# Kernel optimization log

Hardware: AMD Instinct MI355X
Metric: run time of the kernel (lower is better)

The kernel has to match this reference:

```python
import jax, jax.numpy as jnp
import numpy as np

N_IN = 100000
N_OUT = 200000
C_IN = 128
C_OUT = 64
K = 27  # 3x3x3 kernel offsets
M = 100000  # neighbor-map pairs per kernel offset
BN_EPS = 1e-5


def setup_inputs() -> dict:
    key = jax.random.key(0)
    k1, k2, k3, k4 = jax.random.split(key, 4)
    x = jax.random.normal(k1, (N_IN, C_IN), dtype=jnp.float32)
    weight = jax.random.normal(k2, (K, C_IN, C_OUT), dtype=jnp.float32) * (1.0 / np.sqrt(C_IN * K))
    gamma = jnp.ones((C_OUT,), dtype=jnp.float32)
    beta = jnp.zeros((C_OUT,), dtype=jnp.float32)
    in_map = jax.random.randint(k3, (K, M), 0, N_IN, dtype=jnp.int32)
    out_map = jax.random.randint(k4, (K, M), 0, N_OUT, dtype=jnp.int32)
    return {"x": x, "weight": weight, "gamma": gamma, "beta": beta,
            "in_map": in_map, "out_map": out_map}


def sparse_transposed_conv(x, weight, in_map, out_map):
    # gather-GEMM-scatter over K kernel offsets (torchsparse semantics)
    out = jnp.zeros((N_OUT, C_OUT), dtype=x.dtype)

    def body(k, out):
        gathered = x[in_map[k]]                # [M, C_in] irregular gather
        contrib = gathered @ weight[k]         # [M, C_out] small GEMM
        return out.at[out_map[k]].add(contrib) # irregular scatter-add

    return jax.lax.fori_loop(0, K, body, out)


def reference(x, weight, gamma, beta, in_map, out_map):
    out = sparse_transposed_conv(x, weight, in_map, out_map)
    # BatchNorm over points (training-mode batch statistics, biased var)
    mean = jnp.mean(out, axis=0)
    var = jnp.mean(jnp.square(out - mean), axis=0)
    y = (out - mean) * (gamma * jax.lax.rsqrt(var + BN_EPS)) + beta
    return jnp.maximum(y, 0.0)  # ReLU
```

## Files before the change

### kernel.cpp

```cpp
#include <hip/hip_runtime.h>
#include <hip/hip_fp16.h>

#define N_IN   100000
#define N_OUT  200000
#define C_IN   128
#define C_OUT  64
#define NK     27
#define MM     100000
#define BN_EPS 1e-5f

#define TILE_M 128
#define APAD   136

typedef short bf16x8 __attribute__((ext_vector_type(8)));
typedef float f32x4  __attribute__((ext_vector_type(4)));

__device__ __forceinline__ unsigned pack2_bf16(float a, float b) {
  unsigned ua = __float_as_uint(a);
  unsigned ub = __float_as_uint(b);
  ua = (ua + 0x7FFFu + ((ua >> 16) & 1u)) >> 16;
  ub = (ub + 0x7FFFu + ((ub >> 16) & 1u)) & 0xFFFF0000u;
  return ua | ub;
}

__device__ __forceinline__ unsigned pack2_f16(float lo, float hi) {
  __half2 h = __floats2half2_rn(lo, hi);
  return *(unsigned*)&h;
}

__device__ __forceinline__ void pk_atomic_f16(const void* addr, unsigned pw) {
  asm volatile("global_atomic_pk_add_f16 %0, %1, off"
               :: "v"((unsigned long long)addr), "v"(pw) : "memory");
}

__global__ void convert_kernel(const float* __restrict__ x, unsigned* __restrict__ xb,
                               const float* __restrict__ w, unsigned* __restrict__ wt) {
  if (blockIdx.x < 6250) {
    int id = blockIdx.x * 256 + threadIdx.x;
    const float4* xs = (const float4*)x;
    float4 v0 = xs[2 * id];
    float4 v1 = xs[2 * id + 1];
    uint4 o;
    o.x = pack2_bf16(v0.x, v0.y);
    o.y = pack2_bf16(v0.z, v0.w);
    o.z = pack2_bf16(v1.x, v1.y);
    o.w = pack2_bf16(v1.z, v1.w);
    ((uint4*)xb)[id] = o;
  } else {
    int pidx = (blockIdx.x - 6250) * 256 + threadIdx.x;
    int k   = pidx >> 12;
    int rem = pidx & 4095;
    int co  = rem >> 6;
    int ci0 = (rem & 63) * 2;
    const float* wk = w + (size_t)k * C_IN * C_OUT;
    float a = wk[ci0 * C_OUT + co];
    float b = wk[(ci0 + 1) * C_OUT + co];
    wt[pidx] = pack2_bf16(a, b);
  }
}

__global__ __launch_bounds__(256, 4) void scatter3_kernel(
    const uint4* __restrict__ xb,
    const unsigned short* __restrict__ wt,
    const int* __restrict__ in_map,
    const int* __restrict__ out_map,
    unsigned short* __restrict__ acc16)
{
  __shared__ unsigned short Bls[C_OUT * APAD];

  const int t = threadIdx.x;
  const int k = blockIdx.y;
  const int mbase = blockIdx.x * TILE_M;

  {
    const uint4* src = (const uint4*)(wt + (size_t)k * C_OUT * C_IN);
    #pragma unroll
    for (int i = 0; i < 4; ++i) {
      int ch  = t + i * 256;
      int co  = ch >> 4;
      int ci0 = (ch & 15) * 8;
      *(uint4*)&Bls[co * APAD + ci0] = src[ch];
    }
  }

  const int wave = t >> 6;
  const int lane = t & 63;
  const int quad = lane >> 4;
  const int l15  = lane & 15;
  const int rb   = wave * 32;

  const int m0 = mbase + rb + l15;
  const int m1 = m0 + 16;
  const int src0 = (m0 < MM) ? in_map[k * MM + m0] : 0;
  const int src1 = (m1 < MM) ? in_map[k * MM + m1] : 0;
  const uint4* xr0 = xb + (size_t)src0 * 16 + quad;
  const uint4* xr1 = xb + (size_t)src1 * 16 + quad;
  uint4 a0[4], a1[4];
  #pragma unroll
  for (int kk = 0; kk < 4; ++kk) {
    a0[kk] = xr0[kk * 4];
    a1[kk] = xr1[kk * 4];
  }

  __syncthreads();

  f32x4 acc[2][4];
  #pragma unroll
  for (int i = 0; i < 2; ++i)
    #pragma unroll
    for (int j = 0; j < 4; ++j)
      acc[i][j] = (f32x4){0.f, 0.f, 0.f, 0.f};

  #pragma unroll
  for (int kk = 0; kk < 4; ++kk) {
    const int koff = kk * 32 + quad * 8;
    bf16x8 fa0 = *(const bf16x8*)&a0[kk];
    bf16x8 fa1 = *(const bf16x8*)&a1[kk];
    bf16x8 b0 = *(const bf16x8*)&Bls[(l15) * APAD + koff];
    bf16x8 b1 = *(const bf16x8*)&Bls[(16 + l15) * APAD + koff];
    bf16x8 b2 = *(const bf16x8*)&Bls[(32 + l15) * APAD + koff];
    bf16x8 b3 = *(const bf16x8*)&Bls[(48 + l15) * APAD + koff];
    acc[0][0] = __builtin_amdgcn_mfma_f32_16x16x32_bf16(fa0, b0, acc[0][0], 0, 0, 0);
    acc[0][1] = __builtin_amdgcn_mfma_f32_16x16x32_bf16(fa0, b1, acc[0][1], 0, 0, 0);
    acc[0][2] = __builtin_amdgcn_mfma_f32_16x16x32_bf16(fa0, b2, acc[0][2], 0, 0, 0);
    acc[0][3] = __builtin_amdgcn_mfma_f32_16x16x32_bf16(fa0, b3, acc[0][3], 0, 0, 0);
    acc[1][0] = __builtin_amdgcn_mfma_f32_16x16x32_bf16(fa1, b0, acc[1][0], 0, 0, 0);
    acc[1][1] = __builtin_amdgcn_mfma_f32_16x16x32_bf16(fa1, b1, acc[1][1], 0, 0, 0);
    acc[1][2] = __builtin_amdgcn_mfma_f32_16x16x32_bf16(fa1, b2, acc[1][2], 0, 0, 0);
    acc[1][3] = __builtin_amdgcn_mfma_f32_16x16x32_bf16(fa1, b3, acc[1][3], 0, 0, 0);
  }

  const int par = l15 & 1;
  #pragma unroll
  for (int rt = 0; rt < 2; ++rt) {
    int rloc = rb + rt * 16 + quad * 4;
    int mrow = mbase + rloc;
    int4 o4;
    if (mrow + 3 < MM) {
      o4 = *(const int4*)(out_map + (size_t)k * MM + mrow);
    } else {
      o4.x = (mrow + 0 < MM) ? out_map[(size_t)k * MM + mrow + 0] : 0;
      o4.y = (mrow + 1 < MM) ? out_map[(size_t)k * MM + mrow + 1] : 0;
      o4.z = (mrow + 2 < MM) ? out_map[(size_t)k * MM + mrow + 2] : 0;
      o4.w = (mrow + 3 < MM) ? out_map[(size_t)k * MM + mrow + 3] : 0;
    }
    int om4[4] = {o4.x, o4.y, o4.z, o4.w};
    #pragma unroll
    for (int ct = 0; ct < 4; ++ct) {
      f32x4 v = acc[rt][ct];
      int colb = ct * 16 + (l15 & ~1);
      #pragma unroll
      for (int i = 0; i < 4; ++i) {
        float vn = __shfl_xor(v[i], 1);
        float lo = par ? vn : v[i];
        float hi = par ? v[i] : vn;
        unsigned pw = pack2_f16(lo, hi);
        if (((i & 1) == par) && (mrow + i < MM)) {
          const unsigned short* addr = acc16 + (size_t)om4[i] * C_OUT + colb;
          pk_atomic_f16(addr, pw);
        }
      }
    }
  }
}

__global__ __launch_bounds__(256) void scatter_f32_kernel(
    const float* __restrict__ x,
    const unsigned short* __restrict__ wt,
    const int* __restrict__ in_map,
    const int* __restrict__ out_map,
    float* __restrict__ outf)
{
  __shared__ unsigned short Als[TILE_M * APAD];
  __shared__ unsigned short Bls[C_OUT * APAD];
  __shared__ int om[TILE_M];

  const int t = threadIdx.x;
  const int k = blockIdx.y;
  const int mbase = blockIdx.x * TILE_M;

  if (t < TILE_M) {
    int m = mbase + t;
    om[t] = (m < MM) ? out_map[k * MM + m] : 0;
  }
  {
    const uint4* src = (const uint4*)(wt + (size_t)k * C_OUT * C_IN);
    #pragma unroll
    for (int i = 0; i < 4; ++i) {
      int ch  = t + i * 256;
      int co  = ch >> 4;
      int ci0 = (ch & 15) * 8;
      *(uint4*)&Bls[co * APAD + ci0] = src[ch];
    }
  }
  {
    int r    = t >> 1;
    int half = t & 1;
    int m    = mbase + r;
    int src  = (m < MM) ? in_map[k * MM + m] : 0;
    const float4* xr = (const float4*)(x + (size_t)src * C_IN) + half * 16;
    uint2* dst = (uint2*)&Als[r * APAD + half * 64];
    #pragma unroll
    for (int j = 0; j < 16; ++j) {
      float4 v = xr[j];
      dst[j] = make_uint2(pack2_bf16(v.x, v.y), pack2_bf16(v.z, v.w));
    }
  }
  __syncthreads();

  const int wave = t >> 6;
  const int lane = t & 63;
  const int quad = lane >> 4;
  const int l15  = lane & 15;
  const int rb   = wave * 32;

  f32x4 acc[2][4];
  #pragma unroll
  for (int i = 0; i < 2; ++i)
    #pragma unroll
    for (int j = 0; j < 4; ++j)
      acc[i][j] = (f32x4){0.f, 0.f, 0.f, 0.f};

  #pragma unroll
  for (int kk = 0; kk < 4; ++kk) {
    const int koff = kk * 32 + quad * 8;
    bf16x8 a0 = *(const bf16x8*)&Als[(rb + l15) * APAD + koff];
    bf16x8 a1 = *(const bf16x8*)&Als[(rb + 16 + l15) * APAD + koff];
    bf16x8 b0 = *(const bf16x8*)&Bls[(l15) * APAD + koff];
    bf16x8 b1 = *(const bf16x8*)&Bls[(16 + l15) * APAD + koff];
    bf16x8 b2 = *(const bf16x8*)&Bls[(32 + l15) * APAD + koff];
    bf16x8 b3 = *(const bf16x8*)&Bls[(48 + l15) * APAD + koff];
    acc[0][0] = __builtin_amdgcn_mfma_f32_16x16x32_bf16(a0, b0, acc[0][0], 0, 0, 0);
    acc[0][1] = __builtin_amdgcn_mfma_f32_16x16x32_bf16(a0, b1, acc[0][1], 0, 0, 0);
    acc[0][2] = __builtin_amdgcn_mfma_f32_16x16x32_bf16(a0, b2, acc[0][2], 0, 0, 0);
    acc[0][3] = __builtin_amdgcn_mfma_f32_16x16x32_bf16(a0, b3, acc[0][3], 0, 0, 0);
    acc[1][0] = __builtin_amdgcn_mfma_f32_16x16x32_bf16(a1, b0, acc[1][0], 0, 0, 0);
    acc[1][1] = __builtin_amdgcn_mfma_f32_16x16x32_bf16(a1, b1, acc[1][1], 0, 0, 0);
    acc[1][2] = __builtin_amdgcn_mfma_f32_16x16x32_bf16(a1, b2, acc[1][2], 0, 0, 0);
    acc[1][3] = __builtin_amdgcn_mfma_f32_16x16x32_bf16(a1, b3, acc[1][3], 0, 0, 0);
  }

  #pragma unroll
  for (int rt = 0; rt < 2; ++rt) {
    int rloc = rb + rt * 16 + quad * 4;
    int4 o4 = *(const int4*)&om[rloc];
    int mrow = mbase + rloc;
    #pragma unroll
    for (int ct = 0; ct < 4; ++ct) {
      f32x4 v = acc[rt][ct];
      int col = ct * 16 + l15;
      if (mrow + 0 < MM) unsafeAtomicAdd(&outf[(size_t)o4.x * C_OUT + col], v[0]);
      if (mrow + 1 < MM) unsafeAtomicAdd(&outf[(size_t)o4.y * C_OUT + col], v[1]);
      if (mrow + 2 < MM) unsafeAtomicAdd(&outf[(size_t)o4.z * C_OUT + col], v[2]);
      if (mrow + 3 < MM) unsafeAtomicAdd(&outf[(size_t)o4.w * C_OUT + col], v[3]);
    }
  }
}

__global__ __launch_bounds__(256) void stats16_kernel(const unsigned* __restrict__ acc,
                                                      float* __restrict__ ws) {
  __shared__ float red[4][8][32];
  int t = threadIdx.x;
  int w = t & 31, sub = t >> 5;
  float s0 = 0, q0 = 0, s1 = 0, q1 = 0;
  for (int r = blockIdx.x * 8 + sub; r < N_OUT; r += gridDim.x * 8) {
    unsigned u = acc[(size_t)r * 32 + w];
    __half2 h = *(__half2*)&u;
    float a = __low2float(h), b = __high2float(h);
    s0 += a; q0 += a * a; s1 += b; q1 += b * b;
  }
  red[0][sub][w] = s0; red[1][sub][w] = q0;
  red[2][sub][w] = s1; red[3][sub][w] = q1;
  __syncthreads();
  if (t < 32) {
    float S0 = 0, Q0 = 0, S1 = 0, Q1 = 0;
    #pragma unroll
    for (int s = 0; s < 8; ++s) {
      S0 += red[0][s][t]; Q0 += red[1][s][t];
      S1 += red[2][s][t]; Q1 += red[3][s][t];
    }
    unsafeAtomicAdd(&ws[2 * t],      S0);
    unsafeAtomicAdd(&ws[64 + 2 * t], Q0);
    unsafeAtomicAdd(&ws[2 * t + 1],      S1);
    unsafeAtomicAdd(&ws[64 + 2 * t + 1], Q1);
  }
}

__global__ void finalize16_kernel(const uint2* __restrict__ acc,
                                  float* __restrict__ out,
                                  const float* __restrict__ ws) {
  int i = blockIdx.x * 256 + threadIdx.x;
  uint2 u = acc[i];
  __half2 h0 = *(__half2*)&u.x;
  __half2 h1 = *(__half2*)&u.y;
  int c0 = (i & 15) * 4;
  float s0 = ws[128 + c0], s1 = ws[129 + c0], s2 = ws[130 + c0], s3 = ws[131 + c0];
  float b0 = ws[192 + c0], b1 = ws[193 + c0], b2 = ws[194 + c0], b3 = ws[195 + c0];
  float4 v;
  v.x = fmaxf(fmaf(__low2float(h0),  s0, b0), 0.f);
  v.y = fmaxf(fmaf(__high2float(h0), s1, b1), 0.f);
  v.z = fmaxf(fmaf(__low2float(h1),  s2, b2), 0.f);
  v.w = fmaxf(fmaf(__high2float(h1), s3, b3), 0.f);
  ((float4*)out)[i] = v;
}

__global__ void stats_kernel(const float* __restrict__ out, float* __restrict__ ws) {
  __shared__ float ls[4][64];
  __shared__ float ls2[4][64];
  int t = threadIdx.x;
  int c = t & 63, sub = t >> 6;
  float s = 0.f, s2 = 0.f;
  for (int r = blockIdx.x * 4 + sub; r < N_OUT; r += gridDim.x * 4) {
    float v = out[(size_t)r * C_OUT + c];
    s += v; s2 += v * v;
  }
  ls[sub][c] = s; ls2[sub][c] = s2;
  __syncthreads();
  if (t < 64) {
    float ts = ls[0][t] + ls[1][t] + ls[2][t] + ls[3][t];
    float t2 = ls2[0][t] + ls2[1][t] + ls2[2][t] + ls2[3][t];
    unsafeAtomicAdd(&ws[t], ts);
    unsafeAtomicAdd(&ws[64 + t], t2);
  }
}

__global__ void finalize_kernel(float* __restrict__ out, const float* __restrict__ ws) {
  int i = blockIdx.x * 256 + threadIdx.x;
  float4 v = ((const float4*)out)[i];
  int c0 = (i & 15) * 4;
  float s0 = ws[128 + c0], s1 = ws[129 + c0], s2 = ws[130 + c0], s3 = ws[131 + c0];
  float b0 = ws[192 + c0], b1 = ws[193 + c0], b2 = ws[194 + c0], b3 = ws[195 + c0];
  v.x = fmaxf(fmaf(v.x, s0, b0), 0.f);
  v.y = fmaxf(fmaf(v.y, s1, b1), 0.f);
  v.z = fmaxf(fmaf(v.z, s2, b2), 0.f);
  v.w = fmaxf(fmaf(v.w, s3, b3), 0.f);
  ((float4*)out)[i] = v;
}

__global__ void prep_kernel(float* __restrict__ ws,
                            const float* __restrict__ gamma,
                            const float* __restrict__ beta) {
  int c = threadIdx.x;
  float mean = ws[c] * (1.0f / N_OUT);
  float var  = ws[64 + c] * (1.0f / N_OUT) - mean * mean;
  var = fmaxf(var, 0.0f);
  float sc = gamma[c] * rsqrtf(var + BN_EPS);
  ws[128 + c] = sc;
  ws[192 + c] = beta[c] - mean * sc;
}

extern "C" void kernel_launch(void* const* d_in, const int* in_sizes, int n_in,
                              void* d_out, int out_size, void* d_ws, size_t ws_size,
                              hipStream_t stream) {
  const float* x      = (const float*)d_in[0];
  const float* weight = (const float*)d_in[1];
  const float* gamma  = (const float*)d_in[2];
  const float* beta   = (const float*)d_in[3];
  const int* in_map   = (const int*)d_in[4];
  const int* out_map  = (const int*)d_in[5];
  float* out   = (float*)d_out;
  float* stats = (float*)d_ws;

  const size_t WT_OFF  = 4096;
  const size_t XB_OFF  = 1u << 20;
  const size_t XB_SZ   = (size_t)N_IN * C_IN * 2;
  const size_t ACC_OFF = XB_OFF + XB_SZ;
  const size_t ACC_SZ  = (size_t)N_OUT * C_OUT * 2;

  unsigned* wt = (unsigned*)((char*)d_ws + WT_OFF);
  unsigned* xb = (unsigned*)((char*)d_ws + XB_OFF);
  unsigned short* acc16 = (unsigned short*)((char*)d_ws + ACC_OFF);

  dim3 g((MM + TILE_M - 1) / TILE_M, NK);
  hipMemsetAsync(d_ws, 0, 1024, stream);

  if (ws_size >= ACC_OFF + ACC_SZ) {
    hipMemsetAsync(acc16, 0, ACC_SZ, stream);
    convert_kernel<<<6682, 256, 0, stream>>>(x, xb, weight, wt);
    scatter3_kernel<<<g, 256, 0, stream>>>((const uint4*)xb, (const unsigned short*)wt,
                                           in_map, out_map, acc16);
    stats16_kernel<<<1024, 256, 0, stream>>>((const unsigned*)acc16, stats);
    prep_kernel<<<1, 64, 0, stream>>>(stats, gamma, beta);
    finalize16_kernel<<<(N_OUT * C_OUT / 4 + 255) / 256, 256, 0, stream>>>(
        (const uint2*)acc16, out, stats);
  } else {
    hipMemsetAsync(d_out, 0, (size_t)N_OUT * C_OUT * sizeof(float), stream);
    convert_kernel<<<6682, 256, 0, stream>>>(x, xb, weight, wt);
    scatter_f32_kernel<<<g, 256, 0, stream>>>(x, (const unsigned short*)wt,
                                              in_map, out_map, out);
    stats_kernel<<<512, 256, 0, stream>>>(out, stats);
    prep_kernel<<<1, 64, 0, stream>>>(stats, gamma, beta);
    finalize_kernel<<<(N_OUT * C_OUT / 4 + 255) / 256, 256, 0, stream>>>(out, stats);
  }
}
```

Measured before the change: 730.7 us.

## Bucket neighbor pairs by output tile and accumulate in LDS before global atomics

Adds a counting-sort pipeline (histogram, per-tile scan, record scatter) that groups gather/scatter pairs by output tile of 100 rows and kernel offset. A new conv kernel then runs MFMA on 16-row chunks, accumulates into an fp32 LDS tile with workgroup atomics, and flushes once per slice with packed f16 global atomics. This is meant to replace many scattered global f16 atomics with LDS atomics plus fewer coalesced global atomics. The cost is several extra kernels and memsets, a large record buffer, and a fixed per-tile capacity that could overflow if the outputs are unevenly distributed.

After: 1.385 ms. 1.9x slower.

```diff
diff --git a/kernel.cpp b/kernel.cpp
--- a/kernel.cpp
+++ b/kernel.cpp
@@ -12,6 +12,13 @@
 #define TILE_M 128
 #define APAD   136
 
+#define TILE_R 100
+#define NTILE  2000
+#define NSLICE 4
+#define CAP_T  2048
+#define LROW   65
+#define CHCAP  128
+
 typedef short bf16x8 __attribute__((ext_vector_type(8)));
 typedef float f32x4  __attribute__((ext_vector_type(4)));
 
@@ -34,8 +41,9 @@
 }
 
 __global__ void convert_kernel(const float* __restrict__ x, unsigned* __restrict__ xb,
-                               const float* __restrict__ w, unsigned* __restrict__ wt) {
-  if (blockIdx.x < 6250) {
+                               const float* __restrict__ w, unsigned* __restrict__ wt,
+                               unsigned* __restrict__ wt2, int xblocks) {
+  if ((int)blockIdx.x < xblocks) {
     int id = blockIdx.x * 256 + threadIdx.x;
     const float4* xs = (const float4*)x;
     float4 v0 = xs[2 * id];
@@ -47,15 +55,167 @@
     o.w = pack2_bf16(v1.z, v1.w);
     ((uint4*)xb)[id] = o;
   } else {
-    int pidx = (blockIdx.x - 6250) * 256 + threadIdx.x;
+    int pidx = (blockIdx.x - xblocks) * 256 + threadIdx.x;
     int k   = pidx >> 12;
-    int rem = pidx & 4095;
-    int co  = rem >> 6;
-    int ci0 = (rem & 63) * 2;
     const float* wk = w + (size_t)k * C_IN * C_OUT;
-    float a = wk[ci0 * C_OUT + co];
-    float b = wk[(ci0 + 1) * C_OUT + co];
-    wt[pidx] = pack2_bf16(a, b);
+    {
+      int rem = pidx & 4095;
+      int co  = rem >> 6;
+      int ci0 = (rem & 63) * 2;
+      wt[pidx] = pack2_bf16(wk[ci0 * C_OUT + co], wk[(ci0 + 1) * C_OUT + co]);
+    }
+    {
+      int p     = pidx & 3;
+      int lane6 = (pidx >> 2) & 63;
+      int kk    = (pidx >> 8) & 3;
+      int ct    = (pidx >> 10) & 3;
+      int co  = ct * 16 + (lane6 & 15);
+      int ci0 = kk * 32 + (lane6 >> 4) * 8 + p * 2;
+      wt2[pidx] = pack2_bf16(wk[ci0 * C_OUT + co], wk[(ci0 + 1) * C_OUT + co]);
+    }
+  }
+}
+
+__global__ void hist_kernel(const int* __restrict__ out_map, int* __restrict__ cnt) {
+  int m = blockIdx.x * 256 + threadIdx.x;
+  int k = blockIdx.y;
+  if (m < MM) {
+    int o = out_map[k * MM + m];
+    atomicAdd(&cnt[(o / TILE_R) * NK + k], 1);
+  }
+}
+
+__global__ void tile_scan_kernel(const int* __restrict__ cnt,
+                                 int* __restrict__ off,
+                                 int* __restrict__ cur) {
+  int tile = blockIdx.x * 4 + (threadIdx.x >> 6);
+  int lane = threadIdx.x & 63;
+  if (tile >= NTILE) return;
+  int c = 0;
+  if (lane < NK) c = (cnt[tile * NK + lane] + 15) & ~15;
+  int p = c;
+  #pragma unroll
+  for (int d = 1; d < 32; d <<= 1) {
+    int n = __shfl_up(p, d);
+    if (lane >= d) p += n;
+  }
+  int base = tile * CAP_T + p - c;
+  if (lane < NK) { off[tile * 28 + lane] = base; cur[tile * 28 + lane] = base; }
+  if (lane == NK - 1) off[tile * 28 + NK] = base + c;
+}
+
+__global__ void scatter_rec_kernel(const int* __restrict__ in_map,
+                                   const int* __restrict__ out_map,
+                                   int* __restrict__ cur,
+                                   unsigned* __restrict__ rec) {
+  int m = blockIdx.x * 256 + threadIdx.x;
+  int k = blockIdx.y;
+  if (m < MM) {
+    int o = out_map[k * MM + m];
+    int tile = o / TILE_R;
+    int ol = o - tile * TILE_R;
+    int pos = atomicAdd(&cur[tile * 28 + k], 1);
+    rec[pos] = ((unsigned)in_map[k * MM + m] << 7) | (unsigned)ol;
+  }
+}
+
+__global__ __launch_bounds__(256) void conv_slice_kernel(
+    const uint4* __restrict__ xb,
+    const uint4* __restrict__ wt2,
+    const unsigned* __restrict__ rec,
+    const int* __restrict__ off,
+    unsigned short* __restrict__ acc16)
+{
+  __shared__ float Lacc[TILE_R * LROW];
+  __shared__ int chtab[CHCAP];
+  __shared__ int nch_s;
+
+  const int t     = threadIdx.x;
+  const int tile  = blockIdx.x >> 2;
+  const int slice = blockIdx.x & 3;
+  const int wave  = t >> 6;
+  const int lane  = t & 63;
+  const int quad  = lane >> 4;
+  const int l15   = lane & 15;
+
+  for (int i = t; i < TILE_R * LROW; i += 256) Lacc[i] = 0.f;
+
+  if (wave == 0) {
+    int cnt = 0, s0 = 0;
+    if (lane < NK) {
+      s0  = off[tile * 28 + lane];
+      cnt = (off[tile * 28 + lane + 1] - s0) >> 4;
+    }
+    int pos = cnt;
+    #pragma unroll
+    for (int d = 1; d < 32; d <<= 1) {
+      int n = __shfl_up(pos, d);
+      if (lane >= d) pos += n;
+    }
+    int base = pos - cnt;
+    for (int i = 0; i < cnt; ++i)
+      chtab[base + i] = (lane << 24) | ((s0 + (i << 4)) & 0xFFFFFF);
+    if (lane == NK - 1) nch_s = pos;
+  }
+  __syncthreads();
+
+  const int nch = nch_s;
+  const int cs  = (nch * slice) >> 2;
+  const int ce  = (nch * (slice + 1)) >> 2;
+
+  int kcur = -1;
+  bf16x8 B[4][4];
+
+  for (int ci = cs + wave; ci < ce; ci += 4) {
+    unsigned ent = (unsigned)chtab[ci];
+    const int k = (int)(ent >> 24);
+    unsigned r0 = rec[(ent & 0xFFFFFFu) + l15];
+    if (k != kcur) {
+      kcur = k;
+      const uint4* wkp = wt2 + (size_t)k * 1024 + lane;
+      #pragma unroll
+      for (int ct = 0; ct < 4; ++ct)
+        #pragma unroll
+        for (int kk = 0; kk < 4; ++kk)
+          B[ct][kk] = *(const bf16x8*)(wkp + (ct * 4 + kk) * 64);
+    }
+    unsigned row0 = (r0 & 0x80000000u) ? 0u : (r0 >> 7);
+    uint4 a[4];
+    #pragma unroll
+    for (int kk = 0; kk < 4; ++kk) a[kk] = xb[(size_t)row0 * 16 + kk * 4 + quad];
+
+    f32x4 acc0 = (f32x4){0.f,0.f,0.f,0.f};
+    f32x4 acc1 = (f32x4){0.f,0.f,0.f,0.f};
+    f32x4 acc2 = (f32x4){0.f,0.f,0.f,0.f};
+    f32x4 acc3 = (f32x4){0.f,0.f,0.f,0.f};
+    #pragma unroll
+    for (int kk = 0; kk < 4; ++kk) {
+      bf16x8 fa = *(const bf16x8*)&a[kk];
+      acc0 = __builtin_amdgcn_mfma_f32_16x16x32_bf16(fa, B[0][kk], acc0, 0, 0, 0);
+      acc1 = __builtin_amdgcn_mfma_f32_16x16x32_bf16(fa, B[1][kk], acc1, 0, 0, 0);
+      acc2 = __builtin_amdgcn_mfma_f32_16x16x32_bf16(fa, B[2][kk], acc2, 0, 0, 0);
+      acc3 = __builtin_amdgcn_mfma_f32_16x16x32_bf16(fa, B[3][kk], acc3, 0, 0, 0);
+    }
+    #pragma unroll
+    for (int i = 0; i < 4; ++i) {
+      unsigned rr = __shfl(r0, quad * 4 + i);
+      if (!(rr & 0x80000000u)) {
+        float* dst = &Lacc[(rr & 127u) * LROW + l15];
+        __hip_atomic_fetch_add(dst +  0, acc0[i], __ATOMIC_RELAXED, __HIP_MEMORY_SCOPE_WORKGROUP);
+        __hip_atomic_fetch_add(dst + 16, acc1[i], __ATOMIC_RELAXED, __HIP_MEMORY_SCOPE_WORKGROUP);
+        __hip_atomic_fetch_add(dst + 32, acc2[i], __ATOMIC_RELAXED, __HIP_MEMORY_SCOPE_WORKGROUP);
+        __hip_atomic_fetch_add(dst + 48, acc3[i], __ATOMIC_RELAXED, __HIP_MEMORY_SCOPE_WORKGROUP);
+      }
+    }
+  }
+  __syncthreads();
+
+  const size_t obase = (size_t)tile * TILE_R * C_OUT;
+  for (int idx = t; idx < TILE_R * 32; idx += 256) {
+    int r  = idx >> 5;
+    int c2 = (idx & 31) << 1;
+    unsigned pw = pack2_f16(Lacc[r * LROW + c2], Lacc[r * LROW + c2 + 1]);
+    pk_atomic_f16(acc16 + obase + (size_t)r * C_OUT + c2, pw);
   }
 }
 
@@ -362,30 +522,61 @@
   float* stats = (float*)d_ws;
 
   const size_t WT_OFF  = 4096;
-  const size_t XB_OFF  = 1u << 20;
+  const size_t WT2_OFF = 512u * 1024;
+  const size_t CNT_OFF = 1024u * 1024;
+  const size_t OFF_OFF = 1280u * 1024;
+  const size_t CUR_OFF = 1536u * 1024;
+  const size_t XB_OFF  = 2u * 1024 * 1024;
   const size_t XB_SZ   = (size_t)N_IN * C_IN * 2;
-  const size_t ACC_OFF = XB_OFF + XB_SZ;
+  const size_t REC_OFF = 28u * 1024 * 1024;
+  const size_t REC_SZ  = (size_t)NTILE * CAP_T * 4;
   const size_t ACC_SZ  = (size_t)N_OUT * C_OUT * 2;
-
-  unsigned* wt = (unsigned*)((char*)d_ws + WT_OFF);
-  unsigned* xb = (unsigned*)((char*)d_ws + XB_OFF);
-  unsigned short* acc16 = (unsigned short*)((char*)d_ws + ACC_OFF);
-
-  dim3 g((MM + TILE_M - 1) / TILE_M, NK);
+  const size_t ACC_MAIN = 45u * 1024 * 1024;
+  const size_t NEED_MAIN = ACC_MAIN + ACC_SZ;
+  const size_t ACC_S3   = REC_OFF;
+  const size_t NEED_S3  = ACC_S3 + ACC_SZ;
+
+  unsigned* wt  = (unsigned*)((char*)d_ws + WT_OFF);
+  unsigned* wt2 = (unsigned*)((char*)d_ws + WT2_OFF);
+  int* cnt      = (int*)((char*)d_ws + CNT_OFF);
+  int* off      = (int*)((char*)d_ws + OFF_OFF);
+  int* cur      = (int*)((char*)d_ws + CUR_OFF);
+  unsigned* xb  = (unsigned*)((char*)d_ws + XB_OFF);
+  unsigned* rec = (unsigned*)((char*)d_ws + REC_OFF);
+
   hipMemsetAsync(d_ws, 0, 1024, stream);
 
-  if (ws_size >= ACC_OFF + ACC_SZ) {
+  if (ws_size >= NEED_MAIN) {
+    unsigned short* acc16 = (unsigned short*)((char*)d_ws + ACC_MAIN);
+    hipMemsetAsync(cnt, 0, (size_t)NTILE * NK * sizeof(int), stream);
+    hipMemsetAsync(rec, 0x80, REC_SZ, stream);
     hipMemsetAsync(acc16, 0, ACC_SZ, stream);
-    convert_kernel<<<6682, 256, 0, stream>>>(x, xb, weight, wt);
-    scatter3_kernel<<<g, 256, 0, stream>>>((const uint4*)xb, (const unsigned short*)wt,
-                                           in_map, out_map, acc16);
+    convert_kernel<<<6682, 256, 0, stream>>>(x, xb, weight, wt, wt2, 6250);
+    hist_kernel<<<dim3((MM + 255) / 256, NK), 256, 0, stream>>>(out_map, cnt);
+    tile_scan_kernel<<<(NTILE + 3) / 4, 256, 0, stream>>>(cnt, off, cur);
+    scatter_rec_kernel<<<dim3((MM + 255) / 256, NK), 256, 0, stream>>>(
+        in_map, out_map, cur, rec);
+    conv_slice_kernel<<<NTILE * NSLICE, 256, 0, stream>>>((const uint4*)xb,
+        (const uint4*)wt2, rec, off, acc16);
+    stats16_kernel<<<1024, 256, 0, stream>>>((const unsigned*)acc16, stats);
+    prep_kernel<<<1, 64, 0, stream>>>(stats, gamma, beta);
+    finalize16_kernel<<<(N_OUT * C_OUT / 4 + 255) / 256, 256, 0, stream>>>(
+        (const uint2*)acc16, out, stats);
+  } else if (ws_size >= NEED_S3) {
+    unsigned short* acc16 = (unsigned short*)((char*)d_ws + ACC_S3);
+    hipMemsetAsync(acc16, 0, ACC_SZ, stream);
+    convert_kernel<<<6682, 256, 0, stream>>>(x, xb, weight, wt, wt2, 6250);
+    dim3 g((MM + TILE_M - 1) / TILE_M, NK);
+    scatter3_kernel<<<g, 256, 0, stream>>>((const uint4*)xb,
+        (const unsigned short*)wt, in_map, out_map, acc16);
     stats16_kernel<<<1024, 256, 0, stream>>>((const unsigned*)acc16, stats);
     prep_kernel<<<1, 64, 0, stream>>>(stats, gamma, beta);
     finalize16_kernel<<<(N_OUT * C_OUT / 4 + 255) / 256, 256, 0, stream>>>(
         (const uint2*)acc16, out, stats);
   } else {
     hipMemsetAsync(d_out, 0, (size_t)N_OUT * C_OUT * sizeof(float), stream);
-    convert_kernel<<<6682, 256, 0, stream>>>(x, xb, weight, wt);
+    convert_kernel<<<432, 256, 0, stream>>>(x, xb, weight, wt, wt2, 0);
+    dim3 g((MM + TILE_M - 1) / TILE_M, NK);
     scatter_f32_kernel<<<g, 256, 0, stream>>>(x, (const unsigned short*)wt,
                                               in_map, out_map, out);
     stats_kernel<<<512, 256, 0, stream>>>(out, stats);
```
